# Kernel optimization log

Measured on AMD Instinct MI355X. Metric: run time of the kernel, lower is better.

## Reference

```python
import jax, jax.numpy as jnp
import numpy as np

N_NODES = 100000
N_EDGES = 3200000
N_GRAPHS = 2048
D = 256
ATOM_VOCAB = 100
BOND_VOCAB = 10
EPS = 1e-5


def setup_inputs() -> dict:
    key = jax.random.key(0)
    ks = jax.random.split(key, 20)
    inp = {
        "x": jax.random.randint(ks[0], (N_NODES, 9), 0, ATOM_VOCAB),
        "edge_index": jax.random.randint(ks[1], (2, N_EDGES), 0, N_NODES),
        "edge_attr": jax.random.randint(ks[2], (N_EDGES, 3), 0, BOND_VOCAB),
        "batch": jnp.sort(jax.random.randint(ks[3], (N_NODES,), 0, N_GRAPHS)),
        # embedding tables (OGB-style: one table per categorical column, summed)
        "atom_emb": jax.random.normal(ks[4], (9, ATOM_VOCAB, D)) * 0.02,
        "bond_emb1": jax.random.normal(ks[5], (3, BOND_VOCAB, D)) * 0.02,
        "bond_emb2": jax.random.normal(ks[6], (3, BOND_VOCAB, D)) * 0.02,
        # conv1 MLP: Linear(D,2D) -> BN -> ReLU -> Linear(2D,D) -> ReLU
        "c1_w1": jax.random.normal(ks[7], (D, 2 * D)) * (1.0 / np.sqrt(D)),
        "c1_b1": jnp.zeros((2 * D,)),
        "c1_g": jnp.ones((2 * D,)),
        "c1_be": jnp.zeros((2 * D,)),
        "c1_w2": jax.random.normal(ks[8], (2 * D, D)) * (1.0 / np.sqrt(2 * D)),
        "c1_b2": jnp.zeros((D,)),
        # conv2 MLP: Linear(D,D) -> BN -> ReLU -> Linear(D,D) -> ReLU
        "c2_w1": jax.random.normal(ks[9], (D, D)) * (1.0 / np.sqrt(D)),
        "c2_b1": jnp.zeros((D,)),
        "c2_g": jnp.ones((D,)),
        "c2_be": jnp.zeros((D,)),
        "c2_w2": jax.random.normal(ks[10], (D, D)) * (1.0 / np.sqrt(D)),
        "c2_b2": jnp.zeros((D,)),
    }
    return inp


def _batchnorm(z, g, b):
    # BatchNorm1d in training mode: batch statistics over the node axis
    mu = jnp.mean(z, axis=0)
    var = jnp.var(z, axis=0)
    return (z - mu) * jax.lax.rsqrt(var + EPS) * g + b


def _bond_encode(tables, edge_attr):
    # sum of per-column embeddings: [E,3] -> [E,D]
    return jnp.sum(tables[jnp.arange(3)[None, :], edge_attr], axis=1)


def _gin_conv(h, edge_index, e_emb, w1, b1, g, be, w2, b2):
    src, dst = edge_index[0], edge_index[1]
    # message: relu(x_j + edge_emb), aggregate: scatter-add at dst
    m = jax.nn.relu(h[src] + e_emb)                       # [E, D]
    agg = jax.ops.segment_sum(m, dst, num_segments=h.shape[0])
    z = agg + h
    z = jax.nn.relu(_batchnorm(z @ w1 + b1, g, be))
    return jax.nn.relu(z @ w2 + b2)


def reference(x, edge_index, edge_attr, batch,
              atom_emb, bond_emb1, bond_emb2,
              c1_w1, c1_b1, c1_g, c1_be, c1_w2, c1_b2,
              c2_w1, c2_b1, c2_g, c2_be, c2_w2, c2_b2):
    # AtomEncoder: sum of 9 per-column embeddings -> [N, D]
    h = jnp.sum(atom_emb[jnp.arange(9)[None, :], x], axis=1)
    e1 = _bond_encode(bond_emb1, edge_attr)
    h = _gin_conv(h, edge_index, e1, c1_w1, c1_b1, c1_g, c1_be, c1_w2, c1_b2)
    h = jax.nn.relu(h)
    e2 = _bond_encode(bond_emb2, edge_attr)
    h = _gin_conv(h, edge_index, e2, c2_w1, c2_b1, c2_g, c2_be, c2_w2, c2_b2)
    h = jax.nn.relu(h)
    # global add pool over graphs
    return jax.ops.segment_sum(h, batch, num_segments=N_GRAPHS)
```

## Files before the change

kernel.cpp:

```cpp
#include <hip/hip_runtime.h>

#define NN 100000
#define NE 3200000
#define NG 2048
#define DD 256
#define EPSV 1e-5f
#define SCAN_N 100096
#define SCAN_B 391
#define GCH 1568
#define NGCH 64

typedef unsigned int uint32;
typedef unsigned short ushort16;
typedef __attribute__((ext_vector_type(4))) unsigned int uivec4;
typedef __attribute__((ext_vector_type(4))) unsigned short usvec4;
typedef __attribute__((ext_vector_type(4))) float f32x4;
typedef __attribute__((ext_vector_type(8))) short short8_t;

__device__ __forceinline__ float4 ld4(const float* p) {
    return *reinterpret_cast<const float4*>(p);
}
__device__ __forceinline__ float bf2f(ushort16 b) {
    return __uint_as_float((uint32)b << 16);
}

__device__ __forceinline__ uint32 packsplit(float x) {
    uint32 u = __float_as_uint(x);
    uint32 hb = (u + 0x7fffu + ((u >> 16) & 1u)) >> 16;
    float hf = __uint_as_float(hb << 16);
    float lo = x - hf;
    uint32 lb = __float_as_uint(lo) >> 16;
    return hb | (lb << 16);
}

__global__ __launch_bounds__(256) void zero_k(float* __restrict__ p, int n) {
    int i = blockIdx.x * 256 + threadIdx.x;
    if (i < n) p[i] = 0.f;
}

__global__ __launch_bounds__(256) void packmat_k(const float* __restrict__ X,
                                                 uint32* __restrict__ Xp, int n) {
    int i = blockIdx.x * 256 + threadIdx.x;
    if (i < n) Xp[i] = packsplit(X[i]);
}

__global__ __launch_bounds__(256) void atom_embed_k(
    const int* __restrict__ x, const float* __restrict__ emb,
    ushort16* __restrict__ Hh, ushort16* __restrict__ Hl)
{
    int lane = threadIdx.x & 63;
    int n = blockIdx.x * 4 + (threadIdx.x >> 6);
    if (n >= NN) return;
    int c4 = lane * 4;
    float4 acc = make_float4(0.f, 0.f, 0.f, 0.f);
#pragma unroll
    for (int c = 0; c < 9; ++c) {
        int idx = x[n * 9 + c];
        float4 v = ld4(emb + (size_t)(c * 100 + idx) * DD + c4);
        acc.x += v.x; acc.y += v.y; acc.z += v.z; acc.w += v.w;
    }
    float a[4] = {acc.x, acc.y, acc.z, acc.w};
    usvec4 h, l;
#pragma unroll
    for (int j = 0; j < 4; ++j) {
        uint32 u = packsplit(a[j]);
        h[j] = (ushort16)(u & 0xffff);
        l[j] = (ushort16)(u >> 16);
    }
    *reinterpret_cast<usvec4*>(Hh + (size_t)n * DD + c4) = h;
    *reinterpret_cast<usvec4*>(Hl + (size_t)n * DD + c4) = l;
}

__global__ __launch_bounds__(256) void bcomb_k(const float* __restrict__ bond,
                                               float* __restrict__ bcomb)
{
    int combo = blockIdx.x;
    int col = threadIdx.x;
    int b0 = combo % 10, b1 = (combo / 10) % 10, b2 = combo / 100;
    bcomb[(size_t)combo * DD + col] =
        bond[(size_t)b0 * DD + col] +
        bond[(size_t)(10 + b1) * DD + col] +
        bond[(size_t)(20 + b2) * DD + col];
}

__global__ __launch_bounds__(256) void hist_k(const int* __restrict__ ei,
                                              int* __restrict__ cnt)
{
    int e = blockIdx.x * 256 + threadIdx.x;
    if (e < NE) atomicAdd(&cnt[ei[NE + e]], 1);
}

__global__ __launch_bounds__(256) void scan1_k(int* __restrict__ cnt,
                                               int* __restrict__ bsum)
{
    __shared__ int s[2][256];
    int t = threadIdx.x;
    int i = blockIdx.x * 256 + t;
    int v = cnt[i];
    s[0][t] = v;
    __syncthreads();
    int p = 0;
    for (int off = 1; off < 256; off <<= 1) {
        int xv = s[p][t];
        if (t >= off) xv += s[p][t - off];
        s[p ^ 1][t] = xv;
        p ^= 1;
        __syncthreads();
    }
    int inc = s[p][t];
    cnt[i] = inc - v;
    if (t == 255) bsum[blockIdx.x] = inc;
}

__global__ __launch_bounds__(512) void scan2_k(const int* __restrict__ bsum,
                                               int* __restrict__ boff)
{
    __shared__ int s[2][512];
    int t = threadIdx.x;
    int v = (t < SCAN_B) ? bsum[t] : 0;
    s[0][t] = v;
    __syncthreads();
    int p = 0;
    for (int off = 1; off < 512; off <<= 1) {
        int xv = s[p][t];
        if (t >= off) xv += s[p][t - off];
        s[p ^ 1][t] = xv;
        p ^= 1;
        __syncthreads();
    }
    boff[t] = s[p][t] - v;
}

__global__ __launch_bounds__(256) void scan3_k(const int* __restrict__ cnt,
                                               const int* __restrict__ boff,
                                               int* __restrict__ rs,
                                               int* __restrict__ cursor)
{
    int i = blockIdx.x * 256 + threadIdx.x;
    int v = cnt[i] + boff[blockIdx.x];
    rs[i] = v;
    if (i < NN) cursor[i] = v;
}

__global__ __launch_bounds__(256) void scatter_k(const int* __restrict__ ei,
                                                 const int* __restrict__ ea,
                                                 int* __restrict__ cursor,
                                                 int* __restrict__ meta)
{
    int e = blockIdx.x * 256 + threadIdx.x;
    if (e >= NE) return;
    int src = ei[e];
    int dst = ei[NE + e];
    int combo = ea[e * 3 + 0] + 10 * ea[e * 3 + 1] + 100 * ea[e * 3 + 2];
    int pos = atomicAdd(&cursor[dst], 1);
    meta[pos] = (src << 10) | combo;
}

__device__ __forceinline__ void edge_acc(const ushort16* __restrict__ Hh,
                                         const float* __restrict__ bcomb,
                                         int m, int c4,
                                         float& a0, float& a1, float& a2, float& a3)
{
    usvec4 v = *reinterpret_cast<const usvec4*>(Hh + (size_t)(m >> 10) * DD + c4);
    float4 b = ld4(bcomb + (size_t)(m & 1023) * DD + c4);
    a0 += fmaxf(bf2f(v[0]) + b.x, 0.f);
    a1 += fmaxf(bf2f(v[1]) + b.y, 0.f);
    a2 += fmaxf(bf2f(v[2]) + b.z, 0.f);
    a3 += fmaxf(bf2f(v[3]) + b.w, 0.f);
}

__global__ __launch_bounds__(256) void gather_full_k(
    const ushort16* __restrict__ Hh, const ushort16* __restrict__ Hl,
    const float* __restrict__ bcomb,
    const int* __restrict__ rs, const int* __restrict__ meta,
    ushort16* __restrict__ Zh, ushort16* __restrict__ Zl)
{
    int lane = threadIdx.x & 63;
    int n = blockIdx.x * 4 + (threadIdx.x >> 6);
    if (n >= NN) return;
    int c4 = lane * 4;
    usvec4 sh = *reinterpret_cast<const usvec4*>(Hh + (size_t)n * DD + c4);
    usvec4 sl = __builtin_nontemporal_load(
        reinterpret_cast<const usvec4*>(Hl + (size_t)n * DD + c4));
    float a0 = bf2f(sh[0]) + bf2f(sl[0]);
    float a1 = bf2f(sh[1]) + bf2f(sl[1]);
    float a2 = bf2f(sh[2]) + bf2f(sl[2]);
    float a3 = bf2f(sh[3]) + bf2f(sl[3]);
    int lo = rs[n], hi = rs[n + 1];
    int t = lo;
    for (; t + 4 <= hi; t += 4) {
        int m0 = __builtin_nontemporal_load(meta + t);
        int m1 = __builtin_nontemporal_load(meta + t + 1);
        int m2 = __builtin_nontemporal_load(meta + t + 2);
        int m3 = __builtin_nontemporal_load(meta + t + 3);
        edge_acc(Hh, bcomb, m0, c4, a0, a1, a2, a3);
        edge_acc(Hh, bcomb, m1, c4, a0, a1, a2, a3);
        edge_acc(Hh, bcomb, m2, c4, a0, a1, a2, a3);
        edge_acc(Hh, bcomb, m3, c4, a0, a1, a2, a3);
    }
    for (; t < hi; ++t)
        edge_acc(Hh, bcomb, __builtin_nontemporal_load(meta + t), c4, a0, a1, a2, a3);
    float a[4] = {a0, a1, a2, a3};
    usvec4 zh, zl;
#pragma unroll
    for (int j = 0; j < 4; ++j) {
        uint32 u = packsplit(a[j]);
        zh[j] = (ushort16)(u & 0xffff);
        zl[j] = (ushort16)(u >> 16);
    }
    __builtin_nontemporal_store(zh, reinterpret_cast<usvec4*>(Zh + (size_t)n * DD + c4));
    __builtin_nontemporal_store(zl, reinterpret_cast<usvec4*>(Zl + (size_t)n * DD + c4));
}

__global__ __launch_bounds__(256) void gram_mfma_k(
    const ushort16* __restrict__ Zh, const ushort16* __restrict__ Zl,
    float* __restrict__ G)
{
    __shared__ uint32 Ta[32][130];
    __shared__ uint32 Tb[32][130];
    const int tid = threadIdx.x;
    const int lane = tid & 63;
    const int l15 = lane & 15;
    const int l4 = lane >> 4;
    const int wave = tid >> 6;
    const int wm = wave >> 1, wn = wave & 1;
    const int bj = blockIdx.x & 1;
    const int bi = (blockIdx.x >> 1) & 1;
    const int ch = blockIdx.x >> 2;
    const int rbase = ch * GCH;

    f32x4 acc[4][4] = {};

    for (int kt = 0; kt < GCH; kt += 32) {
        __syncthreads();
#pragma unroll
        for (int i = 0; i < 4; ++i) {
            int f = i * 256 + tid;
            int row = f >> 5, g4 = f & 31;
            int r = rbase + kt + row;
            uivec4 pa = {0, 0, 0, 0}, pb = {0, 0, 0, 0};
            if (r < NN) {
                const ushort16* zh = Zh + (size_t)r * DD;
                const ushort16* zl = Zl + (size_t)r * DD;
                usvec4 ah_ = *reinterpret_cast<const usvec4*>(zh + bi * 128 + g4 * 4);
                usvec4 al_ = *reinterpret_cast<const usvec4*>(zl + bi * 128 + g4 * 4);
                usvec4 bh_ = *reinterpret_cast<const usvec4*>(zh + bj * 128 + g4 * 4);
                usvec4 bl_ = *reinterpret_cast<const usvec4*>(zl + bj * 128 + g4 * 4);
#pragma unroll
                for (int j = 0; j < 4; ++j) {
                    pa[j] = (uint32)ah_[j] | ((uint32)al_[j] << 16);
                    pb[j] = (uint32)bh_[j] | ((uint32)bl_[j] << 16);
                }
            }
            *reinterpret_cast<uivec4*>(&Ta[row][g4 * 4]) = pa;
            *reinterpret_cast<uivec4*>(&Tb[row][g4 * 4]) = pb;
        }
        __syncthreads();

        short8_t ah[4], al[4], bh[4], bl[4];
#pragma unroll
        for (int mi = 0; mi < 4; ++mi) {
            int ci = wm * 64 + mi * 16 + l15;
            short8_t h, l;
#pragma unroll
            for (int j = 0; j < 8; ++j) {
                uint32 u = Ta[l4 * 8 + j][ci];
                h[j] = (short)(u & 0xffff);
                l[j] = (short)(u >> 16);
            }
            ah[mi] = h; al[mi] = l;
        }
#pragma unroll
        for (int ni = 0; ni < 4; ++ni) {
            int ci = wn * 64 + ni * 16 + l15;
            short8_t h, l;
#pragma unroll
            for (int j = 0; j < 8; ++j) {
                uint32 u = Tb[l4 * 8 + j][ci];
                h[j] = (short)(u & 0xffff);
                l[j] = (short)(u >> 16);
            }
            bh[ni] = h; bl[ni] = l;
        }
#pragma unroll
        for (int mi = 0; mi < 4; ++mi)
#pragma unroll
            for (int ni = 0; ni < 4; ++ni) {
                acc[mi][ni] = __builtin_amdgcn_mfma_f32_16x16x32_bf16(ah[mi], bh[ni], acc[mi][ni], 0, 0, 0);
                acc[mi][ni] = __builtin_amdgcn_mfma_f32_16x16x32_bf16(ah[mi], bl[ni], acc[mi][ni], 0, 0, 0);
                acc[mi][ni] = __builtin_amdgcn_mfma_f32_16x16x32_bf16(al[mi], bh[ni], acc[mi][ni], 0, 0, 0);
            }
    }

#pragma unroll
    for (int mi = 0; mi < 4; ++mi) {
#pragma unroll
        for (int ni = 0; ni < 4; ++ni) {
            int col = bj * 128 + wn * 64 + ni * 16 + l15;
#pragma unroll
            for (int r = 0; r < 4; ++r) {
                int row = bi * 128 + wm * 64 + mi * 16 + l4 * 4 + r;
                atomicAdd(&G[row * 256 + col], acc[mi][ni][r]);
            }
        }
    }
}

__global__ __launch_bounds__(256) void colsum_k(const ushort16* __restrict__ Zh,
                                                const ushort16* __restrict__ Zl,
                                                float* __restrict__ cs)
{
    int t = threadIdx.x;
    int r0 = blockIdx.x * 256;
    int r1 = r0 + 256 < NN ? r0 + 256 : NN;
    float acc = 0.f;
    for (int r = r0; r < r1; ++r)
        acc += bf2f(Zh[(size_t)r * DD + t]) + bf2f(Zl[(size_t)r * DD + t]);
    atomicAdd(&cs[t], acc);
}

__global__ __launch_bounds__(256) void bnprep_k(
    const float* __restrict__ G, const float* __restrict__ cs,
    const float* __restrict__ W, const float* __restrict__ b,
    const float* __restrict__ g, const float* __restrict__ be,
    float* __restrict__ scl, float* __restrict__ shf, int N)
{
    __shared__ float wv[256];
    __shared__ double r1[256];
    __shared__ double r2[256];
    int c = blockIdx.x;
    int t = threadIdx.x;
    wv[t] = W[t * N + c];
    __syncthreads();
    double gd = 0.0;
    const float* Gr = G + t * 256;
    for (int j = 0; j < 256; ++j) gd += (double)Gr[j] * (double)wv[j];
    r1[t] = (double)wv[t] * gd;
    r2[t] = (double)cs[t] * (double)wv[t];
    __syncthreads();
    for (int off = 128; off > 0; off >>= 1) {
        if (t < off) { r1[t] += r1[t + off]; r2[t] += r2[t + off]; }
        __syncthreads();
    }
    if (t == 0) {
        double szw = r2[0];
        double s2zw = r1[0];
        double bb = (double)b[c];
        double fN = (double)NN;
        double S1 = szw + fN * bb;
        double S2 = s2zw + 2.0 * bb * szw + fN * bb * bb;
        double mu = S1 / fN;
        double var = S2 / fN - mu * mu;
        float s = g[c] * rsqrtf((float)var + EPSV);
        scl[c] = s;
        shf[c] = be[c] - (float)mu * s;
    }
}

template <int OUTM, bool ASPLIT, bool CSPLIT>
__global__ __launch_bounds__(256) void gemm_mfma_k(
    const ushort16* __restrict__ Ah, const ushort16* __restrict__ Al,
    const uint32* __restrict__ Wp, const float* __restrict__ bias,
    ushort16* __restrict__ Ch, ushort16* __restrict__ Cl,
    int M, int N, int K,
    const float* __restrict__ scl, const float* __restrict__ shf)
{
    __shared__ uint32 As[128][36];

    const int tid = threadIdx.x;
    const int lane = tid & 63;
    const int l15 = lane & 15;
    const int l4 = lane >> 4;
    const int wave = tid >> 6;
    const int wm = wave >> 1, wn = wave & 1;
    const int ntx = N / 128;
    const int bx = blockIdx.x % ntx;
    const int by = blockIdx.x / ntx;
    const int row0 = by * 128, col0 = bx * 128;

    f32x4 acc[4][4] = {};

    for (int kt = 0; kt < K; kt += 32) {
        __syncthreads();
#pragma unroll
        for (int i = 0; i < 4; ++i) {
            int f = i * 256 + tid;
            int row = f >> 3, q = f & 7;
            int r = row0 + row;
            if (r >= M) r = M - 1;
            usvec4 hh = *reinterpret_cast<const usvec4*>(Ah + (size_t)r * K + kt + q * 4);
            uivec4 pk;
            if constexpr (ASPLIT) {
                usvec4 ll = *reinterpret_cast<const usvec4*>(Al + (size_t)r * K + kt + q * 4);
#pragma unroll
                for (int j = 0; j < 4; ++j)
                    pk[j] = (uint32)hh[j] | ((uint32)ll[j] << 16);
            } else {
#pragma unroll
                for (int j = 0; j < 4; ++j)
                    pk[j] = (uint32)hh[j];
            }
            *reinterpret_cast<uivec4*>(&As[row][q * 4]) = pk;
        }
        __syncthreads();

        short8_t ah[4], al[4];
#pragma unroll
        for (int mi = 0; mi < 4; ++mi) {
            int m = wm * 64 + mi * 16 + l15;
            uivec4 u0 = *reinterpret_cast<const uivec4*>(&As[m][l4 * 8]);
            uivec4 u1 = *reinterpret_cast<const uivec4*>(&As[m][l4 * 8 + 4]);
            short8_t h, l;
#pragma unroll
            for (int j = 0; j < 4; ++j) {
                h[j] = (short)(u0[j] & 0xffff);
                h[4 + j] = (short)(u1[j] & 0xffff);
                if constexpr (ASPLIT) {
                    l[j] = (short)(u0[j] >> 16);
                    l[4 + j] = (short)(u1[j] >> 16);
                }
            }
            ah[mi] = h;
            if constexpr (ASPLIT) al[mi] = l;
        }
        short8_t bh[4], bl[4];
#pragma unroll
        for (int ni = 0; ni < 4; ++ni) {
            int col = col0 + wn * 64 + ni * 16 + l15;
            const uint32* wp = Wp + (size_t)(kt + l4 * 8) * N + col;
            short8_t h, l;
#pragma unroll
            for (int j = 0; j < 8; ++j) {
                uint32 u = wp[(size_t)j * N];
                h[j] = (short)(u & 0xffff);
                l[j] = (short)(u >> 16);
            }
            bh[ni] = h; bl[ni] = l;
        }
#pragma unroll
        for (int mi = 0; mi < 4; ++mi)
#pragma unroll
            for (int ni = 0; ni < 4; ++ni) {
                acc[mi][ni] = __builtin_amdgcn_mfma_f32_16x16x32_bf16(ah[mi], bh[ni], acc[mi][ni], 0, 0, 0);
                acc[mi][ni] = __builtin_amdgcn_mfma_f32_16x16x32_bf16(ah[mi], bl[ni], acc[mi][ni], 0, 0, 0);
                if constexpr (ASPLIT)
                    acc[mi][ni] = __builtin_amdgcn_mfma_f32_16x16x32_bf16(al[mi], bh[ni], acc[mi][ni], 0, 0, 0);
            }
    }

#pragma unroll
    for (int ni = 0; ni < 4; ++ni) {
        int col = col0 + wn * 64 + ni * 16 + l15;
        float bv = bias[col];
        float sc = 0.f, sh = 0.f;
        if constexpr (OUTM == 2) { sc = scl[col]; sh = shf[col]; }
#pragma unroll
        for (int mi = 0; mi < 4; ++mi) {
#pragma unroll
            for (int r = 0; r < 4; ++r) {
                int row = row0 + wm * 64 + mi * 16 + l4 * 4 + r;
                if (row < M) {
                    float v = acc[mi][ni][r] + bv;
                    if constexpr (OUTM == 2) v = fmaf(v, sc, sh);
                    v = fmaxf(v, 0.f);
                    uint32 u = packsplit(v);
                    Ch[(size_t)row * N + col] = (ushort16)(u & 0xffff);
                    if constexpr (CSPLIT)
                        Cl[(size_t)row * N + col] = (ushort16)(u >> 16);
                }
            }
        }
    }
}

__device__ __forceinline__ int lower_bound_i(const int* a, int n, int key) {
    int lo = 0, hi = n;
    while (lo < hi) {
        int mid = (lo + hi) >> 1;
        if (a[mid] < key) lo = mid + 1; else hi = mid;
    }
    return lo;
}

__global__ __launch_bounds__(256) void pool_k(
    const ushort16* __restrict__ Hh, const ushort16* __restrict__ Hl,
    const int* __restrict__ batch, float* __restrict__ out)
{
    int g = blockIdx.x;
    int col = threadIdx.x;
    int lo = lower_bound_i(batch, NN, g);
    int hi = lower_bound_i(batch, NN, g + 1);
    float acc = 0.f;
    for (int n = lo; n < hi; ++n)
        acc += bf2f(Hh[(size_t)n * DD + col]) + bf2f(Hl[(size_t)n * DD + col]);
    out[(size_t)g * DD + col] = acc;
}

extern "C" void kernel_launch(void* const* d_in, const int* in_sizes, int n_in,
                              void* d_out, int out_size, void* d_ws, size_t ws_size,
                              hipStream_t stream)
{
    const int*   x        = (const int*)d_in[0];
    const int*   ei       = (const int*)d_in[1];
    const int*   ea       = (const int*)d_in[2];
    const int*   batch    = (const int*)d_in[3];
    const float* atom_emb = (const float*)d_in[4];
    const float* bond1    = (const float*)d_in[5];
    const float* bond2    = (const float*)d_in[6];
    const float* c1_w1    = (const float*)d_in[7];
    const float* c1_b1    = (const float*)d_in[8];
    const float* c1_g     = (const float*)d_in[9];
    const float* c1_be    = (const float*)d_in[10];
    const float* c1_w2    = (const float*)d_in[11];
    const float* c1_b2    = (const float*)d_in[12];
    const float* c2_w1    = (const float*)d_in[13];
    const float* c2_b1    = (const float*)d_in[14];
    const float* c2_g     = (const float*)d_in[15];
    const float* c2_be    = (const float*)d_in[16];
    const float* c2_w2    = (const float*)d_in[17];
    const float* c2_b2    = (const float*)d_in[18];
    float* out = (float*)d_out;

    ushort16* Hh = (ushort16*)d_ws;
    ushort16* Hl = Hh + (size_t)NN * DD;
    ushort16* Zh = Hl + (size_t)NN * DD;
    ushort16* Zl = Zh + (size_t)NN * DD;
    float*  G    = (float*)(Zl + (size_t)NN * DD);
    float*  cs   = G + 65536;
    float*  scl  = cs + 256;
    float*  shf  = scl + 512;
    float*  bcomb = shf + 512;
    uint32* W1p = (uint32*)(bcomb + 1000 * DD);
    uint32* W2p = W1p + 256 * 512;
    uint32* W3p = W2p + 512 * 256;
    uint32* W4p = W3p + 256 * 256;
    int* cnt    = (int*)(W4p + 256 * 256);
    int* rs     = cnt + SCAN_N;
    int* bsum   = rs + SCAN_N;
    int* boff   = bsum + 512;
    int* cursor = boff + 512;
    int* meta   = cursor + NN;
    char* ybase = (char*)(meta + NE);

    size_t fixed_bytes = (size_t)(ybase - (char*)d_ws);
    size_t avail = ws_size > fixed_bytes ? ws_size - fixed_bytes : 0;
    int strip = (int)(avail / 1024);
    strip = (strip / 128) * 128;
    if (strip > 100096) strip = 100096;
    if (strip < 128) strip = 128;
    ushort16* ysh = (ushort16*)ybase;

    const int eb = (NE + 255) / 256;

    zero_k<<<(SCAN_N + 255) / 256, 256, 0, stream>>>((float*)cnt, SCAN_N);
    zero_k<<<(65792 + 255) / 256, 256, 0, stream>>>(G, 65792);

    packmat_k<<<512, 256, 0, stream>>>(c1_w1, W1p, 256 * 512);
    packmat_k<<<512, 256, 0, stream>>>(c1_w2, W2p, 512 * 256);
    packmat_k<<<256, 256, 0, stream>>>(c2_w1, W3p, 256 * 256);
    packmat_k<<<256, 256, 0, stream>>>(c2_w2, W4p, 256 * 256);

    atom_embed_k<<<NN / 4, 256, 0, stream>>>(x, atom_emb, Hh, Hl);

    hist_k<<<eb, 256, 0, stream>>>(ei, cnt);
    scan1_k<<<SCAN_B, 256, 0, stream>>>(cnt, bsum);
    scan2_k<<<1, 512, 0, stream>>>(bsum, boff);
    scan3_k<<<SCAN_B, 256, 0, stream>>>(cnt, boff, rs, cursor);
    scatter_k<<<eb, 256, 0, stream>>>(ei, ea, cursor, meta);

    bcomb_k<<<1000, 256, 0, stream>>>(bond1, bcomb);
    gather_full_k<<<NN / 4, 256, 0, stream>>>(Hh, Hl, bcomb, rs, meta, Zh, Zl);
    gram_mfma_k<<<4 * NGCH, 256, 0, stream>>>(Zh, Zl, G);
    colsum_k<<<SCAN_B, 256, 0, stream>>>(Zh, Zl, cs);
    bnprep_k<<<512, 256, 0, stream>>>(G, cs, c1_w1, c1_b1, c1_g, c1_be, scl, shf, 512);
    for (int r0 = 0; r0 < NN; r0 += strip) {
        int Ms = (NN - r0 < strip) ? NN - r0 : strip;
        int mt = (Ms + 127) / 128;
        gemm_mfma_k<2, true, false><<<mt * 4, 256, 0, stream>>>(
            Zh + (size_t)r0 * DD, Zl + (size_t)r0 * DD, W1p, c1_b1,
            ysh, nullptr, Ms, 512, 256, scl, shf);
        gemm_mfma_k<1, false, true><<<mt * 2, 256, 0, stream>>>(
            ysh, nullptr, W2p, c1_b2,
            Hh + (size_t)r0 * DD, Hl + (size_t)r0 * DD, Ms, 256, 512, nullptr, nullptr);
    }

    zero_k<<<(65792 + 255) / 256, 256, 0, stream>>>(G, 65792);
    bcomb_k<<<1000, 256, 0, stream>>>(bond2, bcomb);
    gather_full_k<<<NN / 4, 256, 0, stream>>>(Hh, Hl, bcomb, rs, meta, Zh, Zl);
    gram_mfma_k<<<4 * NGCH, 256, 0, stream>>>(Zh, Zl, G);
    colsum_k<<<SCAN_B, 256, 0, stream>>>(Zh, Zl, cs);
    bnprep_k<<<256, 256, 0, stream>>>(G, cs, c2_w1, c2_b1, c2_g, c2_be, scl, shf, 256);
    for (int r0 = 0; r0 < NN; r0 += strip) {
        int Ms = (NN - r0 < strip) ? NN - r0 : strip;
        int mt = (Ms + 127) / 128;
        gemm_mfma_k<2, true, false><<<mt * 2, 256, 0, stream>>>(
            Zh + (size_t)r0 * DD, Zl + (size_t)r0 * DD, W3p, c2_b1,
            ysh, nullptr, Ms, 256, 256, scl, shf);
        gemm_mfma_k<1, false, true><<<mt * 2, 256, 0, stream>>>(
            ysh, nullptr, W4p, c2_b2,
            Hh + (size_t)r0 * DD, Hl + (size_t)r0 * DD, Ms, 256, 256, nullptr, nullptr);
    }

    pool_k<<<NG, 256, 0, stream>>>(Hh, Hl, batch, out);
}
```

Before: 2.264 ms.

## Register-prefetch next K tile in gram and GEMM kernels, stage weights in LDS

The gram and GEMM kernels now load the next 32-wide K slice into registers while the MFMAs on the current LDS tile run. Each uses a k-contiguous transposed LDS layout so fragments are read as 128-bit vectors instead of scalar strided reads. The GEMM also stages the weight tile through shared memory rather than reading it strided from global memory per wave. In the gather kernel, nontemporal loads and stores are replaced with ordinary ones. The cost is higher register use for the prefetch buffers, which may lower occupancy.

```diff
diff --git a/kernel.cpp b/kernel.cpp
--- a/kernel.cpp
+++ b/kernel.cpp
@@ -13,6 +13,7 @@
 typedef unsigned int uint32;
 typedef unsigned short ushort16;
 typedef __attribute__((ext_vector_type(4))) unsigned int uivec4;
+typedef __attribute__((ext_vector_type(2))) unsigned short usvec2;
 typedef __attribute__((ext_vector_type(4))) unsigned short usvec4;
 typedef __attribute__((ext_vector_type(4))) float f32x4;
 typedef __attribute__((ext_vector_type(8))) short short8_t;
@@ -180,8 +181,7 @@
     if (n >= NN) return;
     int c4 = lane * 4;
     usvec4 sh = *reinterpret_cast<const usvec4*>(Hh + (size_t)n * DD + c4);
-    usvec4 sl = __builtin_nontemporal_load(
-        reinterpret_cast<const usvec4*>(Hl + (size_t)n * DD + c4));
+    usvec4 sl = *reinterpret_cast<const usvec4*>(Hl + (size_t)n * DD + c4);
     float a0 = bf2f(sh[0]) + bf2f(sl[0]);
     float a1 = bf2f(sh[1]) + bf2f(sl[1]);
     float a2 = bf2f(sh[2]) + bf2f(sl[2]);
@@ -189,17 +189,14 @@
     int lo = rs[n], hi = rs[n + 1];
     int t = lo;
     for (; t + 4 <= hi; t += 4) {
-        int m0 = __builtin_nontemporal_load(meta + t);
-        int m1 = __builtin_nontemporal_load(meta + t + 1);
-        int m2 = __builtin_nontemporal_load(meta + t + 2);
-        int m3 = __builtin_nontemporal_load(meta + t + 3);
+        int m0 = meta[t], m1 = meta[t + 1], m2 = meta[t + 2], m3 = meta[t + 3];
         edge_acc(Hh, bcomb, m0, c4, a0, a1, a2, a3);
         edge_acc(Hh, bcomb, m1, c4, a0, a1, a2, a3);
         edge_acc(Hh, bcomb, m2, c4, a0, a1, a2, a3);
         edge_acc(Hh, bcomb, m3, c4, a0, a1, a2, a3);
     }
     for (; t < hi; ++t)
-        edge_acc(Hh, bcomb, __builtin_nontemporal_load(meta + t), c4, a0, a1, a2, a3);
+        edge_acc(Hh, bcomb, meta[t], c4, a0, a1, a2, a3);
     float a[4] = {a0, a1, a2, a3};
     usvec4 zh, zl;
 #pragma unroll
@@ -208,16 +205,16 @@
         zh[j] = (ushort16)(u & 0xffff);
         zl[j] = (ushort16)(u >> 16);
     }
-    __builtin_nontemporal_store(zh, reinterpret_cast<usvec4*>(Zh + (size_t)n * DD + c4));
-    __builtin_nontemporal_store(zl, reinterpret_cast<usvec4*>(Zl + (size_t)n * DD + c4));
+    *reinterpret_cast<usvec4*>(Zh + (size_t)n * DD + c4) = zh;
+    *reinterpret_cast<usvec4*>(Zl + (size_t)n * DD + c4) = zl;
 }
 
 __global__ __launch_bounds__(256) void gram_mfma_k(
     const ushort16* __restrict__ Zh, const ushort16* __restrict__ Zl,
     float* __restrict__ G)
 {
-    __shared__ uint32 Ta[32][130];
-    __shared__ uint32 Tb[32][130];
+    __shared__ uint32 Ta[128][36];
+    __shared__ uint32 Tb[128][36];
     const int tid = threadIdx.x;
     const int lane = tid & 63;
     const int l15 = lane & 15;
@@ -229,56 +226,75 @@
     const int ch = blockIdx.x >> 2;
     const int rbase = ch * GCH;
 
+    const int cp = tid & 63;
+    const int col2 = cp * 2;
+
     f32x4 acc[4][4] = {};
-
+    uivec4 rA0[2], rA1[2], rB0[2], rB1[2];
+
+    auto LOADG = [&](int kt) {
+#pragma unroll
+        for (int i = 0; i < 2; ++i) {
+            int kg = i * 4 + (tid >> 6);
+            uivec4 pa0, pa1, pb0, pb1;
+#pragma unroll
+            for (int jj = 0; jj < 4; ++jj) {
+                int r = rbase + kt + kg * 4 + jj;
+                uint32 va0 = 0, va1 = 0, vb0 = 0, vb1 = 0;
+                if (r < NN) {
+                    size_t ro = (size_t)r * DD;
+                    usvec2 ah_ = *reinterpret_cast<const usvec2*>(Zh + ro + bi * 128 + col2);
+                    usvec2 al_ = *reinterpret_cast<const usvec2*>(Zl + ro + bi * 128 + col2);
+                    usvec2 bh_ = *reinterpret_cast<const usvec2*>(Zh + ro + bj * 128 + col2);
+                    usvec2 bl_ = *reinterpret_cast<const usvec2*>(Zl + ro + bj * 128 + col2);
+                    va0 = (uint32)ah_[0] | ((uint32)al_[0] << 16);
+                    va1 = (uint32)ah_[1] | ((uint32)al_[1] << 16);
+                    vb0 = (uint32)bh_[0] | ((uint32)bl_[0] << 16);
+                    vb1 = (uint32)bh_[1] | ((uint32)bl_[1] << 16);
+                }
+                pa0[jj] = va0; pa1[jj] = va1; pb0[jj] = vb0; pb1[jj] = vb1;
+            }
+            rA0[i] = pa0; rA1[i] = pa1; rB0[i] = pb0; rB1[i] = pb1;
+        }
+    };
+
+    LOADG(0);
     for (int kt = 0; kt < GCH; kt += 32) {
+#pragma unroll
+        for (int i = 0; i < 2; ++i) {
+            int kg = i * 4 + (tid >> 6);
+            *reinterpret_cast<uivec4*>(&Ta[col2][kg * 4])     = rA0[i];
+            *reinterpret_cast<uivec4*>(&Ta[col2 + 1][kg * 4]) = rA1[i];
+            *reinterpret_cast<uivec4*>(&Tb[col2][kg * 4])     = rB0[i];
+            *reinterpret_cast<uivec4*>(&Tb[col2 + 1][kg * 4]) = rB1[i];
+        }
         __syncthreads();
-#pragma unroll
-        for (int i = 0; i < 4; ++i) {
-            int f = i * 256 + tid;
-            int row = f >> 5, g4 = f & 31;
-            int r = rbase + kt + row;
-            uivec4 pa = {0, 0, 0, 0}, pb = {0, 0, 0, 0};
-            if (r < NN) {
-                const ushort16* zh = Zh + (size_t)r * DD;
-                const ushort16* zl = Zl + (size_t)r * DD;
-                usvec4 ah_ = *reinterpret_cast<const usvec4*>(zh + bi * 128 + g4 * 4);
-                usvec4 al_ = *reinterpret_cast<const usvec4*>(zl + bi * 128 + g4 * 4);
-                usvec4 bh_ = *reinterpret_cast<const usvec4*>(zh + bj * 128 + g4 * 4);
-                usvec4 bl_ = *reinterpret_cast<const usvec4*>(zl + bj * 128 + g4 * 4);
-#pragma unroll
-                for (int j = 0; j < 4; ++j) {
-                    pa[j] = (uint32)ah_[j] | ((uint32)al_[j] << 16);
-                    pb[j] = (uint32)bh_[j] | ((uint32)bl_[j] << 16);
-                }
-            }
-            *reinterpret_cast<uivec4*>(&Ta[row][g4 * 4]) = pa;
-            *reinterpret_cast<uivec4*>(&Tb[row][g4 * 4]) = pb;
-        }
-        __syncthreads();
+        if (kt + 32 < GCH) LOADG(kt + 32);
 
         short8_t ah[4], al[4], bh[4], bl[4];
 #pragma unroll
         for (int mi = 0; mi < 4; ++mi) {
             int ci = wm * 64 + mi * 16 + l15;
+            uivec4 u0 = *reinterpret_cast<const uivec4*>(&Ta[ci][l4 * 8]);
+            uivec4 u1 = *reinterpret_cast<const uivec4*>(&Ta[ci][l4 * 8 + 4]);
             short8_t h, l;
 #pragma unroll
-            for (int j = 0; j < 8; ++j) {
-                uint32 u = Ta[l4 * 8 + j][ci];
-                h[j] = (short)(u & 0xffff);
-                l[j] = (short)(u >> 16);
+            for (int j = 0; j < 4; ++j) {
+                h[j] = (short)(u0[j] & 0xffff);     l[j] = (short)(u0[j] >> 16);
+                h[4 + j] = (short)(u1[j] & 0xffff); l[4 + j] = (short)(u1[j] >> 16);
             }
             ah[mi] = h; al[mi] = l;
         }
 #pragma unroll
         for (int ni = 0; ni < 4; ++ni) {
             int ci = wn * 64 + ni * 16 + l15;
+            uivec4 u0 = *reinterpret_cast<const uivec4*>(&Tb[ci][l4 * 8]);
+            uivec4 u1 = *reinterpret_cast<const uivec4*>(&Tb[ci][l4 * 8 + 4]);
             short8_t h, l;
 #pragma unroll
-            for (int j = 0; j < 8; ++j) {
-                uint32 u = Tb[l4 * 8 + j][ci];
-                h[j] = (short)(u & 0xffff);
-                l[j] = (short)(u >> 16);
+            for (int j = 0; j < 4; ++j) {
+                h[j] = (short)(u0[j] & 0xffff);     l[j] = (short)(u0[j] >> 16);
+                h[4 + j] = (short)(u1[j] & 0xffff); l[4 + j] = (short)(u1[j] >> 16);
             }
             bh[ni] = h; bl[ni] = l;
         }
@@ -290,6 +306,7 @@
                 acc[mi][ni] = __builtin_amdgcn_mfma_f32_16x16x32_bf16(ah[mi], bl[ni], acc[mi][ni], 0, 0, 0);
                 acc[mi][ni] = __builtin_amdgcn_mfma_f32_16x16x32_bf16(al[mi], bh[ni], acc[mi][ni], 0, 0, 0);
             }
+        __syncthreads();
     }
 
 #pragma unroll
@@ -366,6 +383,7 @@
     const float* __restrict__ scl, const float* __restrict__ shf)
 {
     __shared__ uint32 As[128][36];
+    __shared__ uint32 Bs[128][36];
 
     const int tid = threadIdx.x;
     const int lane = tid & 63;
@@ -379,9 +397,9 @@
     const int row0 = by * 128, col0 = bx * 128;
 
     f32x4 acc[4][4] = {};
-
-    for (int kt = 0; kt < K; kt += 32) {
-        __syncthreads();
+    uivec4 rA[4], rB[4];
+
+    auto LOADA = [&](int kt) {
 #pragma unroll
         for (int i = 0; i < 4; ++i) {
             int f = i * 256 + tid;
@@ -400,9 +418,34 @@
                 for (int j = 0; j < 4; ++j)
                     pk[j] = (uint32)hh[j];
             }
-            *reinterpret_cast<uivec4*>(&As[row][q * 4]) = pk;
+            rA[i] = pk;
+        }
+    };
+    auto LOADB = [&](int kt) {
+#pragma unroll
+        for (int i = 0; i < 4; ++i) {
+            int f = i * 256 + tid;
+            int col = f & 127, kg = f >> 7;
+            const uint32* wp = Wp + (size_t)(kt + kg * 4) * N + col0 + col;
+            uivec4 w;
+#pragma unroll
+            for (int jj = 0; jj < 4; ++jj) w[jj] = wp[(size_t)jj * N];
+            rB[i] = w;
+        }
+    };
+
+    LOADA(0); LOADB(0);
+    for (int kt = 0; kt < K; kt += 32) {
+#pragma unroll
+        for (int i = 0; i < 4; ++i) {
+            int f = i * 256 + tid;
+            int row = f >> 3, q = f & 7;
+            *reinterpret_cast<uivec4*>(&As[row][q * 4]) = rA[i];
+            int col = f & 127, kg = f >> 7;
+            *reinterpret_cast<uivec4*>(&Bs[col][kg * 4]) = rB[i];
         }
         __syncthreads();
+        if (kt + 32 < K) { LOADA(kt + 32); LOADB(kt + 32); }
 
         short8_t ah[4], al[4];
 #pragma unroll
@@ -426,14 +469,14 @@
         short8_t bh[4], bl[4];
 #pragma unroll
         for (int ni = 0; ni < 4; ++ni) {
-            int col = col0 + wn * 64 + ni * 16 + l15;
-            const uint32* wp = Wp + (size_t)(kt + l4 * 8) * N + col;
+            int ci = wn * 64 + ni * 16 + l15;
+            uivec4 u0 = *reinterpret_cast<const uivec4*>(&Bs[ci][l4 * 8]);
+            uivec4 u1 = *reinterpret_cast<const uivec4*>(&Bs[ci][l4 * 8 + 4]);
             short8_t h, l;
 #pragma unroll
-            for (int j = 0; j < 8; ++j) {
-                uint32 u = wp[(size_t)j * N];
-                h[j] = (short)(u & 0xffff);
-                l[j] = (short)(u >> 16);
+            for (int j = 0; j < 4; ++j) {
+                h[j] = (short)(u0[j] & 0xffff);     l[j] = (short)(u0[j] >> 16);
+                h[4 + j] = (short)(u1[j] & 0xffff); l[4 + j] = (short)(u1[j] >> 16);
             }
             bh[ni] = h; bl[ni] = l;
         }
@@ -446,6 +489,7 @@
                 if constexpr (ASPLIT)
                     acc[mi][ni] = __builtin_amdgcn_mfma_f32_16x16x32_bf16(al[mi], bh[ni], acc[mi][ni], 0, 0, 0);
             }
+        __syncthreads();
     }
 
 #pragma unroll
```

Measured after the change: 2.200 ms. 2.8% less time.
